# Kernel optimization log

Hardware: AMD Instinct MI355X
Metric: run time of the kernel (lower is better)

The kernel has to match this reference:

```python
import jax, jax.numpy as jnp
import numpy as np

B, M, N, K = 128, 32, 64, 2048  # batch, queue rows, strokes per step, stroke length (K <= M*N)


def setup_inputs() -> dict:
    key = jax.random.key(0)
    ks = jax.random.split(key, 18)
    f32 = jnp.float32
    rn = lambda k, s, sc=1.0: jax.random.normal(k, s, f32) * sc
    return {
        'qt1': rn(ks[0], (B, M, N, 2)),
        'ht1': rn(ks[1], (B, N, 2)),
        'zt': rn(ks[2], (B, N)),
        'alpha_t': jax.random.uniform(ks[3], (B, N), f32),
        'conv_w': rn(ks[4], (2, 2, M + 1, 1), 0.1),  # OIHW, kernel (M+1, 1)
        'conv_b': rn(ks[5], (2,), 0.1),
        'W_xr': rn(ks[6], (2, 2)), 'W_hr': rn(ks[7], (2, 2)), 'b_r': rn(ks[8], (2,)),
        'W_xu': rn(ks[9], (2, 2)), 'W_hu': rn(ks[10], (2, 2)), 'b_u': rn(ks[11], (2,)),
        'W_xn': rn(ks[12], (2, 2)), 'W_hn': rn(ks[13], (2, 2)), 'b_n': rn(ks[14], (2,)),
        'lin_w': rn(ks[15], (N, 2 * N), 0.05),
        'lin_b': rn(ks[16], (N,), 0.05),
        'W_emb': rn(ks[17], (K, 2), 0.1),  # stereo stroke waveform table (stands in for embedding_layer)
    }


def reference(qt1, ht1, zt, alpha_t, conv_w, conv_b, W_xr, W_hr, b_r, W_xu, W_hu, b_u, W_xn, W_hn, b_n, lin_w, lin_b, W_emb):
    Bx = qt1.shape[0]
    # memory matrix: queue + hidden state -> [B, M+1, N, 2]
    Mt1 = jnp.concatenate([qt1, ht1[:, None]], axis=1)
    # full-height (M+1,1) conv over 2 channels, position-wise over N -> [B, N, 2]
    Ht1 = jnp.einsum('bhnc,och->bno', Mt1, conv_w[..., 0]) + conv_b
    xt = jnp.stack([zt, alpha_t], axis=-1)  # [B, N, 2]
    # tiny GRU-style gating on the 2-channel state
    rt = jax.nn.sigmoid(xt @ W_xr + Ht1 @ W_hr + b_r)
    ut = jax.nn.sigmoid(xt @ W_xu + Ht1 @ W_hu + b_u)
    nt = jnp.tanh(xt @ W_xn + (rt * Ht1) @ W_hn + b_n)
    ht = ut * ht1 + (1.0 - ut) * nt  # [B, N, 2]
    it = ht.reshape(Bx, 2 * N) @ lin_w.T + lin_b  # [B, N] stroke intensities
    # embedding: intensity-scaled stroke waveform per onset -> [B, N, K, 2]
    srt = (it * alpha_t)[:, :, None, None] * W_emb[None, None]
    # shifted scatter-accumulate (overlap-add): f_srt[:, i:i+K] += srt[:, i]
    pos = (jnp.arange(N)[:, None] + jnp.arange(K)[None, :]).reshape(-1)  # [N*K]
    f_srt = jnp.zeros((Bx, N + K - 1, 2), srt.dtype).at[:, pos].add(srt.reshape(Bx, N * K, 2))
    st = qt1[:, 0] + f_srt[:, :N]  # emitted samples [B, N, 2]
    # shift queue up one row and add the remaining overlap tail into the flattened queue
    q_shift = jnp.concatenate([qt1[:, 1:], jnp.zeros_like(qt1[:, :1])], axis=1).reshape(Bx, M * N, 2)
    tail = jnp.pad(f_srt[:, N:], ((0, 0), (0, M * N - (K - 1)), (0, 0)))
    qt = (q_shift + tail).reshape(Bx, M, N, 2)
    return st, qt, ht
```

## Files before the change

kernel.cpp:

```cpp
#include <hip/hip_runtime.h>
#include <math.h>

#define NB 128
#define NM 32
#define NN 64
#define NK 2048
#define NP (NN + NK - 1)
#define HALF0 1056

__global__ __launch_bounds__(256) void gen_cell_kernel(
    const float* __restrict__ qt1,
    const float* __restrict__ ht1,
    const float* __restrict__ zt,
    const float* __restrict__ alpha_t,
    const float* __restrict__ conv_w,
    const float* __restrict__ conv_b,
    const float* __restrict__ W_xr, const float* __restrict__ W_hr, const float* __restrict__ b_r,
    const float* __restrict__ W_xu, const float* __restrict__ W_hu, const float* __restrict__ b_u,
    const float* __restrict__ W_xn, const float* __restrict__ W_hn, const float* __restrict__ b_n,
    const float* __restrict__ lin_w, const float* __restrict__ lin_b,
    const float* __restrict__ W_emb,
    float* __restrict__ out)
{
    const int b    = blockIdx.x >> 1;
    const int half = blockIdx.x & 1;
    const int tid  = threadIdx.x;

    __shared__ __align__(16) float s_w[2 * NK];
    __shared__ __align__(16) float s_f[2 * HALF0];
    __shared__ __align__(16) float s_ht[2 * NN];
    __shared__ float s_s[NN];

    {
        const float4* src = (const float4*)W_emb;
        float4* dst = (float4*)s_w;
        #pragma unroll
        for (int i = 0; i < 4; ++i) dst[tid + 256 * i] = src[tid + 256 * i];
    }

    float* st_out = out;
    float* qt_out = out + NB * NN * 2;
    float* ht_out = out + NB * NN * 2 + NB * NM * NN * 2;

    if (tid < NN) {
        const int n = tid;
        const float* q = qt1 + (size_t)b * (NM * NN * 2) + n * 2;
        float h0 = conv_b[0], h1 = conv_b[1];
        #pragma unroll
        for (int h = 0; h < NM; ++h) {
            float m0 = q[h * (NN * 2)];
            float m1 = q[h * (NN * 2) + 1];
            h0 = fmaf(m0, conv_w[h],      fmaf(m1, conv_w[33 + h], h0));
            h1 = fmaf(m0, conv_w[66 + h], fmaf(m1, conv_w[99 + h], h1));
        }
        const float hp0 = ht1[b * (NN * 2) + n * 2];
        const float hp1 = ht1[b * (NN * 2) + n * 2 + 1];
        h0 = fmaf(hp0, conv_w[32],      fmaf(hp1, conv_w[33 + 32], h0));
        h1 = fmaf(hp0, conv_w[66 + 32], fmaf(hp1, conv_w[99 + 32], h1));

        const float x0 = zt[b * NN + n];
        const float x1 = alpha_t[b * NN + n];

        float pr0 = x0*W_xr[0] + x1*W_xr[2] + h0*W_hr[0] + h1*W_hr[2] + b_r[0];
        float pr1 = x0*W_xr[1] + x1*W_xr[3] + h0*W_hr[1] + h1*W_hr[3] + b_r[1];
        float r0 = 1.f / (1.f + expf(-pr0));
        float r1 = 1.f / (1.f + expf(-pr1));

        float pu0 = x0*W_xu[0] + x1*W_xu[2] + h0*W_hu[0] + h1*W_hu[2] + b_u[0];
        float pu1 = x0*W_xu[1] + x1*W_xu[3] + h0*W_hu[1] + h1*W_hu[3] + b_u[1];
        float u0 = 1.f / (1.f + expf(-pu0));
        float u1 = 1.f / (1.f + expf(-pu1));

        float g0 = r0 * h0, g1 = r1 * h1;
        float pn0 = x0*W_xn[0] + x1*W_xn[2] + g0*W_hn[0] + g1*W_hn[2] + b_n[0];
        float pn1 = x0*W_xn[1] + x1*W_xn[3] + g0*W_hn[1] + g1*W_hn[3] + b_n[1];
        float nt0 = tanhf(pn0);
        float nt1 = tanhf(pn1);

        float ho0 = u0 * hp0 + (1.f - u0) * nt0;
        float ho1 = u1 * hp1 + (1.f - u1) * nt1;
        s_ht[n * 2]     = ho0;
        s_ht[n * 2 + 1] = ho1;
        if (half == 0) {
            ht_out[b * (NN * 2) + n * 2]     = ho0;
            ht_out[b * (NN * 2) + n * 2 + 1] = ho1;
        }
    }
    __syncthreads();

    if (tid < NN) {
        const int n = tid;
        float acc = lin_b[n];
        const float4* lw4 = (const float4*)(lin_w + n * (2 * NN));
        const float4* h4  = (const float4*)s_ht;
        #pragma unroll
        for (int j = 0; j < 32; ++j) {
            float4 lw = lw4[j];
            float4 hv = h4[j];
            acc = fmaf(lw.x, hv.x, acc);
            acc = fmaf(lw.y, hv.y, acc);
            acc = fmaf(lw.z, hv.z, acc);
            acc = fmaf(lw.w, hv.w, acc);
        }
        s_s[n] = acc * alpha_t[b * NN + n];
    }
    __syncthreads();

    const int plo = half ? HALF0 : 0;
    const int phi = half ? NP : HALF0;
    const float2* w2 = (const float2*)s_w;
    for (int p = plo + tid; p < phi; p += 256) {
        int nlo = p - (NK - 1); nlo = nlo < 0 ? 0 : nlo;
        int nhi = p < NN - 1 ? p : NN - 1;
        float a0 = 0.f, a1 = 0.f;
        for (int n = nlo; n <= nhi; ++n) {
            float sv = s_s[n];
            float2 wv = w2[p - n];
            a0 = fmaf(sv, wv.x, a0);
            a1 = fmaf(sv, wv.y, a1);
        }
        s_f[(p - plo) * 2]     = a0;
        s_f[(p - plo) * 2 + 1] = a1;
    }
    __syncthreads();

    if (half == 0 && tid < 128) {
        st_out[b * 128 + tid] = qt1[(size_t)b * 4096 + tid] + s_f[tid];
    }
    {
        const float* qb = qt1 + (size_t)b * 4096;
        float* ob = qt_out + (size_t)b * 4096;
        const int ilo = half ? 496 : 0;
        const int ihi = half ? 1024 : 496;
        const int fofs = 128 - 2 * plo;
        for (int i = ilo + tid; i < ihi; i += 256) {
            int x = i * 4;
            float4 v;
            if (x <= 3964) {
                const float4 qv = *(const float4*)(qb + 128 + x);
                const float4 fv = *(const float4*)(s_f + fofs + x);
                v.x = qv.x + fv.x; v.y = qv.y + fv.y;
                v.z = qv.z + fv.z; v.w = qv.w + fv.w;
            } else {
                float tmp[4];
                #pragma unroll
                for (int c = 0; c < 4; ++c) {
                    int xx = x + c;
                    float qv = (xx < 3968) ? qb[128 + xx] : 0.f;
                    float fv = (xx < 4094) ? s_f[fofs + xx] : 0.f;
                    tmp[c] = qv + fv;
                }
                v.x = tmp[0]; v.y = tmp[1]; v.z = tmp[2]; v.w = tmp[3];
            }
            *(float4*)(ob + x) = v;
        }
    }
}

extern "C" void kernel_launch(void* const* d_in, const int* in_sizes, int n_in,
                              void* d_out, int out_size, void* d_ws, size_t ws_size,
                              hipStream_t stream) {
    (void)in_sizes; (void)n_in; (void)out_size; (void)d_ws; (void)ws_size;
    gen_cell_kernel<<<dim3(NB * 2), dim3(256), 0, stream>>>(
        (const float*)d_in[0],  (const float*)d_in[1],  (const float*)d_in[2],
        (const float*)d_in[3],  (const float*)d_in[4],  (const float*)d_in[5],
        (const float*)d_in[6],  (const float*)d_in[7],  (const float*)d_in[8],
        (const float*)d_in[9],  (const float*)d_in[10], (const float*)d_in[11],
        (const float*)d_in[12], (const float*)d_in[13], (const float*)d_in[14],
        (const float*)d_in[15], (const float*)d_in[16], (const float*)d_in[17],
        (float*)d_out);
}
```

Before: 111.0 us.

## Use zero-padded reversed stroke table for branchless fixed-trip convolution

Stores W_emb reversed in shared memory with zero padding at both ends. Every output position can then run a fixed 64-iteration inner loop with no per-position bounds. Each thread computes four positions in one pass, sharing the s_s load, plus a short tail loop for the remaining 32 positions per half. This removes loop-bound divergence and variable trip counts. In exchange, edge positions do extra multiply-by-zero work and shared-memory use rises slightly.

```diff
diff --git a/kernel.cpp b/kernel.cpp
--- a/kernel.cpp
+++ b/kernel.cpp
@@ -7,6 +7,7 @@
 #define NK 2048
 #define NP (NN + NK - 1)
 #define HALF0 1056
+#define NR 2176
 
 __global__ __launch_bounds__(256) void gen_cell_kernel(
     const float* __restrict__ qt1,
@@ -26,16 +27,18 @@
     const int half = blockIdx.x & 1;
     const int tid  = threadIdx.x;
 
-    __shared__ __align__(16) float s_w[2 * NK];
+    __shared__ __align__(16) float2 s_wr[NR];
     __shared__ __align__(16) float s_f[2 * HALF0];
     __shared__ __align__(16) float s_ht[2 * NN];
     __shared__ float s_s[NN];
 
     {
-        const float4* src = (const float4*)W_emb;
-        float4* dst = (float4*)s_w;
-        #pragma unroll
-        for (int i = 0; i < 4; ++i) dst[tid + 256 * i] = src[tid + 256 * i];
+        const float2* w2g = (const float2*)W_emb;
+        float2 z2; z2.x = 0.f; z2.y = 0.f;
+        for (int i = tid; i < NR; i += 256) {
+            float2 v = (i >= 64 && i < 2112) ? w2g[NP - i] : z2;
+            s_wr[i] = v;
+        }
     }
 
     float* st_out = out;
@@ -107,20 +110,44 @@
     __syncthreads();
 
     const int plo = half ? HALF0 : 0;
-    const int phi = half ? NP : HALF0;
-    const float2* w2 = (const float2*)s_w;
-    for (int p = plo + tid; p < phi; p += 256) {
-        int nlo = p - (NK - 1); nlo = nlo < 0 ? 0 : nlo;
-        int nhi = p < NN - 1 ? p : NN - 1;
-        float a0 = 0.f, a1 = 0.f;
-        for (int n = nlo; n <= nhi; ++n) {
+    {
+        const int p0 = plo + tid;
+        const float2* R0 = s_wr + (NP - p0);
+        const float2* R1 = R0 - 256;
+        const float2* R2p = R0 - 512;
+        const float2* R3 = R0 - 768;
+        float a00 = 0.f, a01 = 0.f, a10 = 0.f, a11 = 0.f;
+        float a20 = 0.f, a21 = 0.f, a30 = 0.f, a31 = 0.f;
+        #pragma unroll 8
+        for (int n = 0; n < NN; ++n) {
             float sv = s_s[n];
-            float2 wv = w2[p - n];
-            a0 = fmaf(sv, wv.x, a0);
-            a1 = fmaf(sv, wv.y, a1);
+            float2 w0 = R0[n];
+            float2 w1 = R1[n];
+            float2 w2v = R2p[n];
+            float2 w3 = R3[n];
+            a00 = fmaf(sv, w0.x, a00); a01 = fmaf(sv, w0.y, a01);
+            a10 = fmaf(sv, w1.x, a10); a11 = fmaf(sv, w1.y, a11);
+            a20 = fmaf(sv, w2v.x, a20); a21 = fmaf(sv, w2v.y, a21);
+            a30 = fmaf(sv, w3.x, a30); a31 = fmaf(sv, w3.y, a31);
         }
-        s_f[(p - plo) * 2]     = a0;
-        s_f[(p - plo) * 2 + 1] = a1;
+        s_f[tid * 2]              = a00; s_f[tid * 2 + 1]              = a01;
+        s_f[(tid + 256) * 2]      = a10; s_f[(tid + 256) * 2 + 1]      = a11;
+        s_f[(tid + 512) * 2]      = a20; s_f[(tid + 512) * 2 + 1]      = a21;
+        s_f[(tid + 768) * 2]      = a30; s_f[(tid + 768) * 2 + 1]      = a31;
+        if (tid < 32) {
+            const int p = plo + 1024 + tid;
+            const float2* Rt = s_wr + (NP - p);
+            float t0 = 0.f, t1 = 0.f;
+            #pragma unroll 8
+            for (int n = 0; n < NN; ++n) {
+                float sv = s_s[n];
+                float2 wv = Rt[n];
+                t0 = fmaf(sv, wv.x, t0);
+                t1 = fmaf(sv, wv.y, t1);
+            }
+            s_f[(1024 + tid) * 2]     = t0;
+            s_f[(1024 + tid) * 2 + 1] = t1;
+        }
     }
     __syncthreads();
 
```

Measured after the change: 100.3 us. 9.7% less time.
